# Optimization experiments

Hardware: AMD Instinct MI355X
Metric: run time of the kernel (lower is better)

Reference implementation:

```python
import jax, jax.numpy as jnp
import numpy as np

B, T, D = 8, 1024, 1024          # batch, time, input_dim
HEADS = 4
K_DIM = 256
HALF = K_DIM // 2                # 128: each sub-key half
N_KEYS = 1024                    # per-half sub-keys -> N_KEYS**2 = 1,048,576 memory slots
KNN = 32                         # top-k
V_DIM = 32                       # compressed_dim (value dim)


def setup_inputs() -> dict:
    key = jax.random.key(0)
    ks = jax.random.split(key, 6)
    x = jax.random.normal(ks[0], (B, T, D), jnp.float32)
    W_q = jax.random.normal(ks[1], (D, HEADS * K_DIM), jnp.float32) / np.float32(np.sqrt(D))
    b_q = jnp.zeros((HEADS * K_DIM,), jnp.float32)
    keys = jax.random.normal(ks[2], (HEADS, 2, N_KEYS, HALF), jnp.float32) / np.float32(np.sqrt(HALF))
    values = jax.random.normal(ks[3], (N_KEYS * N_KEYS, V_DIM), jnp.float32) / np.float32(np.sqrt(V_DIM))
    W_r = jax.random.normal(ks[4], (V_DIM, D), jnp.float32) / np.float32(np.sqrt(V_DIM))
    b_r = jnp.zeros((D,), jnp.float32)
    return {"x": x, "W_q": W_q, "b_q": b_q, "keys": keys, "values": values, "W_r": W_r, "b_r": b_r}


def reference(x, W_q, b_q, keys, values, W_r, b_r):
    N = B * T
    xf = x.reshape(N, D)
    # query projection -> (N, heads, 2, half)
    q = (xf @ W_q + b_q).reshape(N, HEADS, 2, HALF)
    # sub-key scores against both half codebooks: (N, H, 2, n_keys)
    scores = jnp.einsum('nhcd,hckd->nhck', q, keys)
    s1, i1 = jax.lax.top_k(scores[:, :, 0], KNN)   # (N,H,KNN)
    s2, i2 = jax.lax.top_k(scores[:, :, 1], KNN)
    # cartesian product of selected sub-keys: (N, H, KNN*KNN)
    comb = (s1[..., :, None] + s2[..., None, :]).reshape(N, HEADS, KNN * KNN)
    idx = (i1[..., :, None] * N_KEYS + i2[..., None, :]).reshape(N, HEADS, KNN * KNN)
    best_s, best_pos = jax.lax.top_k(comb, KNN)    # (N,H,KNN)
    best_idx = jnp.take_along_axis(idx, best_pos, axis=-1)
    w = jax.nn.softmax(best_s, axis=-1)
    # sparse value lookup + per-sample-weighted sum (EmbeddingBag 'sum'), then sum over heads
    vals = values[best_idx]                        # (N,H,KNN,V_DIM) irregular gather
    y = jnp.einsum('nhk,nhkv->nv', w, vals)        # (N, V_DIM)
    out = xf + y @ W_r + b_r                       # reproj + residual
    return out.reshape(B, T, D)
```

## Files before the change

kernel.cpp:

```cpp
#include <hip/hip_runtime.h>
#include <hip/hip_bf16.h>

#define NTOK   8192
#define DDIM   1024
#define NHEADS 4
#define KDIM   256
#define HALF   128
#define NKEYS  1024
#define KNN    32
#define VDIM   32
#define CHUNK  1024

typedef __attribute__((ext_vector_type(8))) short bf16x8;
typedef __attribute__((ext_vector_type(4))) float f32x4;

__device__ __forceinline__ unsigned short f2bf(float f) {
  __hip_bfloat16 h = __float2bfloat16(f);
  return *reinterpret_cast<unsigned short*>(&h);
}

#define GLOAD_LDS16(g, l)                                             \
  __builtin_amdgcn_global_load_lds(                                   \
      (const __attribute__((address_space(1))) void*)(g),             \
      (__attribute__((address_space(3))) void*)(l), 16, 0, 0)

__global__ __launch_bounds__(256) void cvt_bf16(const float* __restrict__ in,
                                                unsigned short* __restrict__ out, int n4) {
  int i = blockIdx.x * 256 + threadIdx.x;
  if (i >= n4) return;
  const float4 v = reinterpret_cast<const float4*>(in)[i];
  ushort4 o;
  o.x = f2bf(v.x); o.y = f2bf(v.y); o.z = f2bf(v.z); o.w = f2bf(v.w);
  reinterpret_cast<ushort4*>(out)[i] = o;
}

__global__ __launch_bounds__(256) void transpose_cvt(const float* __restrict__ W,
                                                     unsigned short* __restrict__ Wt) {
  __shared__ float t[64][65];
  const int bi = blockIdx.y, bj = blockIdx.x;
  const int tid = threadIdx.x;
  const int col = tid & 63;
#pragma unroll
  for (int p = 0; p < 16; p++) {
    const int row = p * 4 + (tid >> 6);
    t[row][col] = W[(size_t)(bi * 64 + row) * DDIM + bj * 64 + col];
  }
  __syncthreads();
#pragma unroll
  for (int p = 0; p < 16; p++) {
    const int row = p * 4 + (tid >> 6);
    Wt[(size_t)(bj * 64 + row) * DDIM + bi * 64 + col] = f2bf(t[col][row]);
  }
}

template <bool OBF, bool BIAS, bool PKM>
__global__ __launch_bounds__(256) void gemm_mfma(const unsigned short* __restrict__ A,
                                                 const unsigned short* __restrict__ B,
                                                 const float* __restrict__ bias,
                                                 void* __restrict__ Cv,
                                                 int K, int lda, int ldb, int ldc,
                                                 long sAz, long sBz, long sCz) {
  __shared__ unsigned short As[128 * 32];
  __shared__ unsigned short Bs[128 * 32];
  size_t Coff;
  if (PKM) {
    const int ch = blockIdx.z >> 3, hc = blockIdx.z & 7;
    A += (size_t)ch * CHUNK * DDIM + (size_t)hc * HALF;
    B += (size_t)hc * ((size_t)NKEYS * HALF);
    Coff = (size_t)ch * CHUNK * (NHEADS * 2 * NKEYS) + (size_t)hc * NKEYS;
  } else {
    A += (size_t)blockIdx.z * sAz;
    B += (size_t)blockIdx.z * sBz;
    Coff = (size_t)blockIdx.z * (size_t)sCz;
  }
  const int tid = threadIdx.x, lane = tid & 63, wv = tid >> 6;
  const int wr = wv >> 1, wc = wv & 1;
  const size_t bm = (size_t)blockIdx.x * 128;
  const size_t bn = (size_t)blockIdx.y * 128;

  const int c0 = tid, c1 = tid + 256;
  const int r0 = c0 >> 2, k0c = (c0 & 3) * 8;
  const int r1 = c1 >> 2, k1c = (c1 & 3) * 8;
  const unsigned short* Ap0 = A + (bm + r0) * (size_t)lda + k0c;
  const unsigned short* Ap1 = A + (bm + r1) * (size_t)lda + k1c;
  const unsigned short* Bp0 = B + (bn + r0) * (size_t)ldb + k0c;
  const unsigned short* Bp1 = B + (bn + r1) * (size_t)ldb + k1c;
  unsigned short* lA0 = As + (size_t)(wv * 64) * 8;
  unsigned short* lA1 = As + (size_t)(wv * 64 + 256) * 8;
  unsigned short* lB0 = Bs + (size_t)(wv * 64) * 8;
  unsigned short* lB1 = Bs + (size_t)(wv * 64 + 256) * 8;

  f32x4 acc[4][4];
#pragma unroll
  for (int m = 0; m < 4; m++)
#pragma unroll
    for (int n = 0; n < 4; n++) acc[m][n] = (f32x4){0.f, 0.f, 0.f, 0.f};

  const int fr = lane & 15;
  const int fk = lane >> 4;

  for (int kt = 0; kt < K; kt += 32) {
    __syncthreads();
    GLOAD_LDS16(Ap0 + kt, lA0);
    GLOAD_LDS16(Ap1 + kt, lA1);
    GLOAD_LDS16(Bp0 + kt, lB0);
    GLOAD_LDS16(Bp1 + kt, lB1);
    __syncthreads();

    bf16x8 af[4], bfv[4];
#pragma unroll
    for (int m = 0; m < 4; m++)
      af[m] = *reinterpret_cast<const bf16x8*>(&As[(wr * 64 + m * 16 + fr) * 32 + fk * 8]);
#pragma unroll
    for (int n = 0; n < 4; n++)
      bfv[n] = *reinterpret_cast<const bf16x8*>(&Bs[(wc * 64 + n * 16 + fr) * 32 + fk * 8]);
#pragma unroll
    for (int m = 0; m < 4; m++)
#pragma unroll
      for (int n = 0; n < 4; n++)
        acc[m][n] = __builtin_amdgcn_mfma_f32_16x16x32_bf16(af[m], bfv[n], acc[m][n], 0, 0, 0);
  }

#pragma unroll
  for (int n = 0; n < 4; n++) {
    const size_t col = bn + wc * 64 + n * 16 + fr;
    const float bv = BIAS ? bias[col] : 0.f;
#pragma unroll
    for (int m = 0; m < 4; m++) {
#pragma unroll
      for (int q = 0; q < 4; q++) {
        const size_t row = bm + wr * 64 + m * 16 + fk * 4 + q;
        const float val = acc[m][n][q] + bv;
        const size_t o = Coff + row * (size_t)ldc + col;
        if (OBF) ((unsigned short*)Cv)[o] = f2bf(val);
        else     ((float*)Cv)[o] = val;
      }
    }
  }
}

__global__ __launch_bounds__(256) void topk_subkeys(const float* __restrict__ sc,
                                                    float* __restrict__ sv,
                                                    int* __restrict__ si) {
  const int lane = threadIdx.x & 63;
  const int gl = blockIdx.x * 4 + (threadIdx.x >> 6);
  const float* s = sc + (size_t)gl * 1024;

  unsigned key[16];
#pragma unroll
  for (int c = 0; c < 4; c++) {
    const float4 f = reinterpret_cast<const float4*>(s)[lane * 4 + c];
    const float ff[4] = {f.x, f.y, f.z, f.w};
#pragma unroll
    for (int e = 0; e < 4; e++) {
      unsigned u = __float_as_uint(ff[e]);
      u = (u & 0x80000000u) ? ~u : (u | 0x80000000u);
      key[c * 4 + e] = (u & 0xFFFFFC00u) | (unsigned)(1023 - (lane * 16 + c * 4 + e));
    }
  }

#pragma unroll
  for (int k = 2; k <= 16; k <<= 1) {
#pragma unroll
    for (int j = k >> 1; j > 0; j >>= 1) {
#pragma unroll
      for (int i = 0; i < 16; i++) {
        const int l = i ^ j;
        if (l > i) {
          const unsigned a = key[i], b = key[l];
          const unsigned hi = a > b ? a : b, lo = a > b ? b : a;
          const bool desc = ((i & k) == 0);
          key[i] = desc ? hi : lo;
          key[l] = desc ? lo : hi;
        }
      }
    }
  }

  float* svp = sv + (size_t)gl * KNN;
  int* sip = si + (size_t)gl * KNN;

#pragma unroll 1
  for (int it = 0; it < KNN; it++) {
    unsigned w = key[0];
#pragma unroll
    for (int off = 1; off < 64; off <<= 1) {
      const unsigned o = __shfl_xor(w, off);
      w = o > w ? o : w;
    }
    const int gidx = 1023 - (int)(w & 1023u);
    if (lane == 0) {
      const unsigned u = w & 0xFFFFFC00u;
      svp[it] = (u & 0x80000000u) ? __uint_as_float(u ^ 0x80000000u)
                                  : __uint_as_float(~u);
      sip[it] = gidx;
    }
    const bool me = (lane == (gidx >> 4));
#pragma unroll
    for (int j = 0; j < 15; j++) key[j] = me ? key[j + 1] : key[j];
    key[15] = me ? 0u : key[15];
  }
}

__device__ const short CAND[128] = {
  0,1,2,3,4,5,6,7,8,9,10,11,12,13,14,15,16,17,18,19,20,21,22,23,24,25,26,27,28,29,30,31,
  32,33,34,35,36,37,38,39,40,41,42,43,44,45,46,47,
  64,65,66,67,68,69,70,71,72,73,
  96,97,98,99,100,101,102,103,
  128,129,130,131,132,133,
  160,161,162,163,164,
  192,193,194,195,
  224,225,226,227,
  256,257,258, 288,289,290,
  320,321, 352,353, 384,385, 416,417, 448,449, 480,481,
  512,544,576,608,640,672,704,736,768,800,832,864,896,928,960,992,
  -1,-1,-1,-1,-1,-1,-1,-1,-1
};

__global__ __launch_bounds__(256) void combine_topk2(const float* __restrict__ sv,
                                                     const int* __restrict__ si,
                                                     const float* __restrict__ values,
                                                     float* __restrict__ y) {
  const int n = blockIdx.x;
  const int w = threadIdx.x >> 6;
  const int lane = threadIdx.x & 63;

  __shared__ float s1v[4][32], s2v[4][32];
  __shared__ int s1i[4][32], s2i[4][32];
  __shared__ float yh[4][32];

  const size_t g1 = ((size_t)(n * 8 + w * 2)) * KNN;
  const size_t g2 = g1 + KNN;
  if (lane < 32) {
    s1v[w][lane] = sv[g1 + lane];
    s1i[w][lane] = si[g1 + lane];
  } else {
    s2v[w][lane - 32] = sv[g2 + lane - 32];
    s2i[w][lane - 32] = si[g2 + lane - 32];
  }

  int id0 = CAND[lane], id1 = CAND[64 + lane];
  float v0 = (id0 < 0) ? -3e38f : s1v[w][id0 >> 5] + s2v[w][id0 & 31];
  float v1 = (id1 < 0) ? -3e38f : s1v[w][id1 >> 5] + s2v[w][id1 & 31];

#pragma unroll
  for (int kb = 1; kb <= 7; ++kb) {
    const int k = 1 << kb;
#pragma unroll
    for (int jb = kb - 1; jb >= 0; --jb) {
      const int j = 1 << jb;
      if (j == 64) {
        if (v1 > v0) {
          const float tv = v0; v0 = v1; v1 = tv;
          const int ti = id0; id0 = id1; id1 = ti;
        }
      } else {
        {
          const int e = lane;
          const float ov = __shfl_xor(v0, j);
          const int oi = __shfl_xor(id0, j);
          const bool up = (e & k) != 0;
          const bool low = (e & j) == 0;
          const bool take = (low != up) ? (ov > v0) : (ov < v0);
          v0 = take ? ov : v0;
          id0 = take ? oi : id0;
        }
        {
          const int e = 64 + lane;
          const float ov = __shfl_xor(v1, j);
          const int oi = __shfl_xor(id1, j);
          const bool up = (e & k) != 0;
          const bool low = (e & j) == 0;
          const bool take = (low != up) ? (ov > v1) : (ov < v1);
          v1 = take ? ov : v1;
          id1 = take ? oi : id1;
        }
      }
    }
  }

  const float m = __shfl(v0, 0);
  const float ev = __expf(v0 - m);
  float es = ev;
#pragma unroll
  for (int off = 16; off; off >>= 1) es += __shfl_xor(es, off);

  const int c0 = (id0 < 0) ? 0 : id0;
  const int mi = s1i[w][c0 >> 5] * NKEYS + s2i[w][c0 & 31];

  const int g = lane >> 5, d = lane & 31;
  float acc = 0.f;
#pragma unroll
  for (int it = 0; it < 16; it++) {
    const int combo = 2 * it + g;
    const float wgt = __shfl(ev, combo);
    const int midx = __shfl(mi, combo);
    acc += wgt * values[(size_t)midx * VDIM + d];
  }
  acc += __shfl_xor(acc, 32);
  if (lane < 32) yh[w][d] = acc / es;
  __syncthreads();
  if (w == 0 && lane < 32) {
    y[(size_t)n * VDIM + lane] = yh[0][lane] + yh[1][lane] + yh[2][lane] + yh[3][lane];
  }
}

__global__ __launch_bounds__(256) void out_proj(const float* __restrict__ x,
                                                const float* __restrict__ yv,
                                                const float* __restrict__ Wr,
                                                const float* __restrict__ br,
                                                float* __restrict__ out) {
  const int nb = blockIdx.x * 8;
  const int t = threadIdx.x;
  __shared__ float ys[8][VDIM];
  ys[t >> 5][t & 31] = yv[(size_t)nb * VDIM + t];
  __syncthreads();

#pragma unroll
  for (int rep = 0; rep < 4; rep++) {
    const int d = t + rep * 256;
    float wcol[VDIM];
#pragma unroll
    for (int vv = 0; vv < VDIM; vv++) wcol[vv] = Wr[vv * DDIM + d];
    const float bb = br[d];
#pragma unroll 1
    for (int tok = 0; tok < 8; tok++) {
      float a = bb;
#pragma unroll
      for (int vv = 0; vv < VDIM; vv++) a = fmaf(ys[tok][vv], wcol[vv], a);
      const size_t o = (size_t)(nb + tok) * DDIM + d;
      out[o] = x[o] + a;
    }
  }
}

extern "C" void kernel_launch(void* const* d_in, const int* in_sizes, int n_in,
                              void* d_out, int out_size, void* d_ws, size_t ws_size,
                              hipStream_t stream) {
  const float* x      = (const float*)d_in[0];
  const float* W_q    = (const float*)d_in[1];
  const float* b_q    = (const float*)d_in[2];
  const float* keys   = (const float*)d_in[3];
  const float* values = (const float*)d_in[4];
  const float* W_r    = (const float*)d_in[5];
  const float* b_r    = (const float*)d_in[6];
  float* out = (float*)d_out;

  unsigned short* qb    = (unsigned short*)d_ws;
  unsigned short* xb    = qb + (size_t)NTOK * DDIM;
  unsigned short* Wqt   = xb + (size_t)NTOK * DDIM;
  unsigned short* keysb = Wqt + (size_t)DDIM * DDIM;
  float* sv = (float*)(keysb + (size_t)NHEADS * 2 * NKEYS * HALF);
  int*   si = (int*)(sv + (size_t)NTOK * NHEADS * 2 * KNN);
  float* y  = (float*)(si + (size_t)NTOK * NHEADS * 2 * KNN);
  float* sc = y + (size_t)NTOK * VDIM;

  cvt_bf16<<<(NTOK * DDIM / 4 + 255) / 256, 256, 0, stream>>>(x, xb, NTOK * DDIM / 4);
  cvt_bf16<<<(NHEADS * 2 * NKEYS * HALF / 4 + 255) / 256, 256, 0, stream>>>(
      keys, keysb, NHEADS * 2 * NKEYS * HALF / 4);
  transpose_cvt<<<dim3(16, 16), 256, 0, stream>>>(W_q, Wqt);

  gemm_mfma<true, true, false><<<dim3(NTOK / 128, DDIM / 128, 1), 256, 0, stream>>>(
      xb, Wqt, b_q, qb, DDIM, DDIM, DDIM, DDIM, 0, 0, 0);

  gemm_mfma<false, false, true><<<dim3(CHUNK / 128, NKEYS / 128, (NTOK / CHUNK) * NHEADS * 2),
                                  256, 0, stream>>>(
      qb, keysb, nullptr, sc, HALF, DDIM, HALF, NHEADS * 2 * NKEYS, 0, 0, 0);

  topk_subkeys<<<NTOK * NHEADS * 2 / 4, 256, 0, stream>>>(sc, sv, si);

  combine_topk2<<<NTOK, 256, 0, stream>>>(sv, si, values, y);

  out_proj<<<NTOK / 8, 256, 0, stream>>>(x, y, W_r, b_r, out);
}
```

Measured before the change: 510.0 us.

## Store sub-key scores as bf16 and pack top-k keys with LDS-backed selection

The score GEMM now writes bf16 instead of fp32, which halves the traffic of the large score buffer between the GEMM and the top-k kernel. The top-k kernel packs the 16-bit ordered score and the index into one 32-bit key. It replaces the per-iteration register shift with an LDS queue of sorted keys read through a head pointer, and emits the packed keys directly. The combine kernel decodes them. This loses score precision to bf16, which could change tie ordering and selection relative to fp32.

```diff
diff --git a/kernel.cpp b/kernel.cpp
--- a/kernel.cpp
+++ b/kernel.cpp
@@ -17,6 +17,12 @@
 __device__ __forceinline__ unsigned short f2bf(float f) {
   __hip_bfloat16 h = __float2bfloat16(f);
   return *reinterpret_cast<unsigned short*>(&h);
+}
+
+__device__ __forceinline__ float dec_key(unsigned k) {
+  const unsigned ord = (k >> 10) & 0xFFFFu;
+  const unsigned v16 = (ord & 0x8000u) ? (ord ^ 0x8000u) : (ord ^ 0xFFFFu);
+  return __uint_as_float(v16 << 16);
 }
 
 #define GLOAD_LDS16(g, l)                                             \
@@ -139,23 +145,27 @@
   }
 }
 
-__global__ __launch_bounds__(256) void topk_subkeys(const float* __restrict__ sc,
-                                                    float* __restrict__ sv,
-                                                    int* __restrict__ si) {
+__global__ __launch_bounds__(256) void topk_subkeys(const unsigned short* __restrict__ sc,
+                                                    unsigned* __restrict__ ski) {
+  __shared__ unsigned heads[4][17][64];
   const int lane = threadIdx.x & 63;
-  const int gl = blockIdx.x * 4 + (threadIdx.x >> 6);
-  const float* s = sc + (size_t)gl * 1024;
+  const int wv = threadIdx.x >> 6;
+  const int gl = blockIdx.x * 4 + wv;
+  const unsigned* s32 = (const unsigned*)(sc + (size_t)gl * 1024 + lane * 16);
 
   unsigned key[16];
-#pragma unroll
-  for (int c = 0; c < 4; c++) {
-    const float4 f = reinterpret_cast<const float4*>(s)[lane * 4 + c];
-    const float ff[4] = {f.x, f.y, f.z, f.w};
-#pragma unroll
-    for (int e = 0; e < 4; e++) {
-      unsigned u = __float_as_uint(ff[e]);
-      u = (u & 0x80000000u) ? ~u : (u | 0x80000000u);
-      key[c * 4 + e] = (u & 0xFFFFFC00u) | (unsigned)(1023 - (lane * 16 + c * 4 + e));
+  {
+    const uint4 p0 = reinterpret_cast<const uint4*>(s32)[0];
+    const uint4 p1 = reinterpret_cast<const uint4*>(s32)[1];
+    const unsigned wds[8] = {p0.x, p0.y, p0.z, p0.w, p1.x, p1.y, p1.z, p1.w};
+    const int base = 1023 - lane * 16;
+#pragma unroll
+    for (int c = 0; c < 8; c++) {
+      unsigned lo = wds[c] & 0xFFFFu, hi = wds[c] >> 16;
+      lo = (lo & 0x8000u) ? (lo ^ 0xFFFFu) : (lo | 0x8000u);
+      hi = (hi & 0x8000u) ? (hi ^ 0xFFFFu) : (hi | 0x8000u);
+      key[2 * c]     = (lo << 10) | (unsigned)(base - 2 * c);
+      key[2 * c + 1] = (hi << 10) | (unsigned)(base - 2 * c - 1);
     }
   }
 
@@ -177,28 +187,27 @@
     }
   }
 
-  float* svp = sv + (size_t)gl * KNN;
-  int* sip = si + (size_t)gl * KNN;
+#pragma unroll
+  for (int j = 1; j < 16; j++) heads[wv][j][lane] = key[j];
+  heads[wv][16][lane] = 0u;
+
+  unsigned h = key[0];
+  int ptr = 1;
+  unsigned* op = ski + (size_t)gl * KNN;
 
 #pragma unroll 1
   for (int it = 0; it < KNN; it++) {
-    unsigned w = key[0];
+    const unsigned nxt = heads[wv][ptr][lane];
+    unsigned w = h;
 #pragma unroll
     for (int off = 1; off < 64; off <<= 1) {
       const unsigned o = __shfl_xor(w, off);
       w = o > w ? o : w;
     }
-    const int gidx = 1023 - (int)(w & 1023u);
-    if (lane == 0) {
-      const unsigned u = w & 0xFFFFFC00u;
-      svp[it] = (u & 0x80000000u) ? __uint_as_float(u ^ 0x80000000u)
-                                  : __uint_as_float(~u);
-      sip[it] = gidx;
-    }
-    const bool me = (lane == (gidx >> 4));
-#pragma unroll
-    for (int j = 0; j < 15; j++) key[j] = me ? key[j + 1] : key[j];
-    key[15] = me ? 0u : key[15];
+    if (lane == 0) op[it] = w;
+    const bool me = (h == w);
+    h = me ? nxt : h;
+    ptr += me ? 1 : 0;
   }
 }
 
@@ -217,8 +226,7 @@
   -1,-1,-1,-1,-1,-1,-1,-1,-1
 };
 
-__global__ __launch_bounds__(256) void combine_topk2(const float* __restrict__ sv,
-                                                     const int* __restrict__ si,
+__global__ __launch_bounds__(256) void combine_topk2(const unsigned* __restrict__ ski,
                                                      const float* __restrict__ values,
                                                      float* __restrict__ y) {
   const int n = blockIdx.x;
@@ -231,12 +239,12 @@
 
   const size_t g1 = ((size_t)(n * 8 + w * 2)) * KNN;
   const size_t g2 = g1 + KNN;
-  if (lane < 32) {
-    s1v[w][lane] = sv[g1 + lane];
-    s1i[w][lane] = si[g1 + lane];
-  } else {
-    s2v[w][lane - 32] = sv[g2 + lane - 32];
-    s2i[w][lane - 32] = si[g2 + lane - 32];
+  {
+    const unsigned kk = ski[(lane < 32) ? (g1 + lane) : (g2 + lane - 32)];
+    const float val = dec_key(kk);
+    const int idx = 1023 - (int)(kk & 1023u);
+    if (lane < 32) { s1v[w][lane] = val; s1i[w][lane] = idx; }
+    else           { s2v[w][lane - 32] = val; s2i[w][lane - 32] = idx; }
   }
 
   int id0 = CAND[lane], id1 = CAND[64 + lane];
@@ -350,10 +358,9 @@
   unsigned short* xb    = qb + (size_t)NTOK * DDIM;
   unsigned short* Wqt   = xb + (size_t)NTOK * DDIM;
   unsigned short* keysb = Wqt + (size_t)DDIM * DDIM;
-  float* sv = (float*)(keysb + (size_t)NHEADS * 2 * NKEYS * HALF);
-  int*   si = (int*)(sv + (size_t)NTOK * NHEADS * 2 * KNN);
-  float* y  = (float*)(si + (size_t)NTOK * NHEADS * 2 * KNN);
-  float* sc = y + (size_t)NTOK * VDIM;
+  unsigned* ski = (unsigned*)(keysb + (size_t)NHEADS * 2 * NKEYS * HALF);
+  float* y = (float*)(ski + (size_t)NTOK * NHEADS * 2 * KNN);
+  unsigned short* sc = (unsigned short*)(y + (size_t)NTOK * VDIM);
 
   cvt_bf16<<<(NTOK * DDIM / 4 + 255) / 256, 256, 0, stream>>>(x, xb, NTOK * DDIM / 4);
   cvt_bf16<<<(NHEADS * 2 * NKEYS * HALF / 4 + 255) / 256, 256, 0, stream>>>(
@@ -363,13 +370,13 @@
   gemm_mfma<true, true, false><<<dim3(NTOK / 128, DDIM / 128, 1), 256, 0, stream>>>(
       xb, Wqt, b_q, qb, DDIM, DDIM, DDIM, DDIM, 0, 0, 0);
 
-  gemm_mfma<false, false, true><<<dim3(CHUNK / 128, NKEYS / 128, (NTOK / CHUNK) * NHEADS * 2),
-                                  256, 0, stream>>>(
+  gemm_mfma<true, false, true><<<dim3(CHUNK / 128, NKEYS / 128, (NTOK / CHUNK) * NHEADS * 2),
+                                 256, 0, stream>>>(
       qb, keysb, nullptr, sc, HALF, DDIM, HALF, NHEADS * 2 * NKEYS, 0, 0, 0);
 
-  topk_subkeys<<<NTOK * NHEADS * 2 / 4, 256, 0, stream>>>(sc, sv, si);
-
-  combine_topk2<<<NTOK, 256, 0, stream>>>(sv, si, values, y);
+  topk_subkeys<<<NTOK * NHEADS * 2 / 4, 256, 0, stream>>>(sc, ski);
+
+  combine_topk2<<<NTOK, 256, 0, stream>>>(ski, values, y);
 
   out_proj<<<NTOK / 8, 256, 0, stream>>>(x, y, W_r, b_r, out);
 }
```

Measured after the change: 493.0 us. -3.3%, faster.
